# Kernel optimization log

Hardware: AMD Instinct MI355X
Metric: run time of the kernel (lower is better)

Reference implementation:

```python
import jax, jax.numpy as jnp
import numpy as np

ALPHA = 0.2  # LeakyReLU negative slope
NEG_BIG = -9e15

def setup_inputs() -> dict:
    key = jax.random.key(0)
    k1, k2, k3, k4, k5 = jax.random.split(key, 5)
    N, IN, OUT = 12288, 512, 256
    inp = jax.random.normal(k1, (N, IN), dtype=jnp.float32)
    adj = jax.random.randint(k2, (N, N), 0, 2, dtype=jnp.int32)
    # xavier_uniform with gain=1.414
    def xavier(k, shape, gain=1.414):
        fan_in, fan_out = shape[0], shape[1]
        bound = gain * np.sqrt(6.0 / (fan_in + fan_out))
        return jax.random.uniform(k, shape, dtype=jnp.float32, minval=-bound, maxval=bound)
    W = xavier(k3, (IN, OUT))
    a1 = xavier(k4, (OUT, 1))
    a2 = xavier(k5, (OUT, 1))
    return {"inp": inp, "adj": adj, "W": W, "a1": a1, "a2": a2}

def reference(inp, adj, W, a1, a2):
    h = inp @ W                      # [N, OUT]
    s1 = h @ a1                      # [N, 1]
    s2 = h @ a2                      # [N, 1]
    e = jax.nn.leaky_relu(s1 + s2.T, negative_slope=ALPHA)   # [N, N]
    scores = jnp.where(adj > 0, e, NEG_BIG)
    attention = jax.nn.softmax(scores, axis=1)               # row-wise softmax
    # dropout is identity in eval mode (training=False)
    h_prime = attention @ h          # [N, OUT]
    return jax.nn.elu(h_prime)       # concat=True -> elu
```

## Files before the change

kernel.cpp:

```cpp
#include <hip/hip_runtime.h>
#include <stdint.h>
#include <stddef.h>

#define NN    12288
#define INF   512
#define OUTF  256
#define ALPHA 0.2f
#define LOG2E 1.44269504088896340736f

typedef __attribute__((ext_vector_type(4))) float        f32x4;
typedef __attribute__((ext_vector_type(8))) short        bf16x8;
typedef __attribute__((ext_vector_type(4))) unsigned int u32x4;
typedef __attribute__((ext_vector_type(4))) int          i32x4;

static __device__ __forceinline__ unsigned short f2bf(float f) {
  union { float f; unsigned u; } v; v.f = f;
  unsigned r = v.u + 0x7fffu + ((v.u >> 16) & 1u);
  return (unsigned short)(r >> 16);
}
static __device__ __forceinline__ float bf2f(unsigned short s) {
  union { unsigned u; float f; } v; v.u = ((unsigned)s) << 16;
  return v.f;
}


__global__ __launch_bounds__(256) void k1_gemm_h(const float* __restrict__ inp,
                                                 const float* __restrict__ W,
                                                 unsigned short* __restrict__ hT) {
  __shared__ float inp_s[32][36];
  __shared__ float W_s[32][256];
  const int t = threadIdx.x;
  const int row0 = blockIdx.x * 32;
  const int tx = t & 63, ty = t >> 6;
  f32x4 acc[8];
#pragma unroll
  for (int r = 0; r < 8; ++r) acc[r] = f32x4{0.f, 0.f, 0.f, 0.f};
  for (int kc = 0; kc < 16; ++kc) {
    {
      const int r = t >> 3, ko = (t & 7) * 4;
      *(f32x4*)&inp_s[r][ko] = *(const f32x4*)(inp + (size_t)(row0 + r) * INF + kc * 32 + ko);
    }
#pragma unroll
    for (int j = 0; j < 8; ++j) {
      const int r = j * 4 + ty;
      *(f32x4*)&W_s[r][tx * 4] = *(const f32x4*)(W + (size_t)(kc * 32 + r) * OUTF + tx * 4);
    }
    __syncthreads();
#pragma unroll 4
    for (int k = 0; k < 32; ++k) {
      const f32x4 wv = *(const f32x4*)&W_s[k][tx * 4];
#pragma unroll
      for (int rr = 0; rr < 8; ++rr) acc[rr] += inp_s[ty * 8 + rr][k] * wv;
    }
    __syncthreads();
  }
#pragma unroll
  for (int rr = 0; rr < 8; ++rr) *(f32x4*)&W_s[ty * 8 + rr][tx * 4] = acc[rr];
  __syncthreads();
  {
    const int col = t;
    char* dst = (char*)hT + (size_t)col * (NN * 2) + (size_t)(row0 >> 6) * 128;
    const unsigned swz = (unsigned)((col & 7) << 4);
    const unsigned wbase = (unsigned)(row0 & 63) * 2;
#pragma unroll
    for (int s = 0; s < 4; ++s) {
      unsigned e0 = (unsigned)f2bf(W_s[s*8+0][col]) | ((unsigned)f2bf(W_s[s*8+1][col]) << 16);
      unsigned e1 = (unsigned)f2bf(W_s[s*8+2][col]) | ((unsigned)f2bf(W_s[s*8+3][col]) << 16);
      unsigned e2 = (unsigned)f2bf(W_s[s*8+4][col]) | ((unsigned)f2bf(W_s[s*8+5][col]) << 16);
      unsigned e3 = (unsigned)f2bf(W_s[s*8+6][col]) | ((unsigned)f2bf(W_s[s*8+7][col]) << 16);
      u32x4 p; p.x = e0; p.y = e1; p.z = e2; p.w = e3;
      *(u32x4*)(dst + ((wbase + (unsigned)s * 16) ^ swz)) = p;
    }
  }
}

__global__ __launch_bounds__(256) void k2_s12(const unsigned short* __restrict__ hT,
                                              const float* __restrict__ a1,
                                              const float* __restrict__ a2,
                                              float* __restrict__ s1,
                                              float* __restrict__ s2) {
  const int i = blockIdx.x * 256 + threadIdx.x;
  const size_t chunk = (size_t)(i >> 6) * 128;
  const unsigned within = (unsigned)(i & 63) * 2;
  float v1 = 0.f, v2 = 0.f;
  for (int d = 0; d < 256; ++d) {
    const unsigned off = within ^ ((unsigned)(d & 7) << 4);
    const unsigned short u =
        *(const unsigned short*)((const char*)hT + (size_t)d * (NN * 2) + chunk + off);
    const float f = bf2f(u);
    v1 += f * a1[d];
    v2 += f * a2[d];
  }
  s1[i] = v1; s2[i] = v2;
}

__global__ __launch_bounds__(256) void k3_s2max(const float* __restrict__ s2,
                                                float* __restrict__ s2max) {
  __shared__ float red[256];
  const int t = threadIdx.x;
  float m = -3.0e38f;
  for (int j = t; j < NN; j += 256) m = fmaxf(m, s2[j]);
  red[t] = m;
  __syncthreads();
  for (int s = 128; s > 0; s >>= 1) {
    if (t < s) red[t] = fmaxf(red[t], red[t + s]);
    __syncthreads();
  }
  if (t == 0) s2max[0] = red[0];
}

__global__ __launch_bounds__(256, 2) void k4_attn(const int* __restrict__ adj,
                                                  const unsigned short* __restrict__ hT,
                                                  const float* __restrict__ s1,
                                                  const float* __restrict__ s2,
                                                  const float* __restrict__ s2max,
                                                  float* __restrict__ accp,
                                                  float* __restrict__ denp) {
  __shared__ __align__(16) char B_lds[256 * 128];
  __shared__ __align__(16) char w_lds[64 * 128];
  const int t = threadIdx.x;
  const int w = t >> 6, l = t & 63;
  const int rb = blockIdx.x >> 1, half = blockIdx.x & 1;
  const int row0 = rb * 64;
  const int kstart = half * (NN / 2);

  const float S2MAX = s2max[0];
  const int wrow = w * 16 + (l >> 2);
  const int wrow_g = row0 + wrow;
  const int k0 = (l & 3) * 16;
  const float s1v = s1[wrow_g];
  const float tup = s1v + S2MAX;
  const float M = tup > 0.f ? tup : ALPHA * tup;
  float dsum = 0.f;

  f32x4 acc[4][4];
#pragma unroll
  for (int i = 0; i < 4; ++i)
#pragma unroll
    for (int j = 0; j < 4; ++j) acc[i][j] = f32x4{0.f, 0.f, 0.f, 0.f};

  const int* adjp = adj + (size_t)wrow_g * NN + kstart + k0;
  const float* s2p = s2 + kstart + k0;
  char* const wdst = w_lds + wrow * 128;
  const unsigned wswz = (unsigned)((wrow & 7) << 4);

  for (int it = 0; it < (NN / 2) / 64; ++it) {
    __syncthreads();
    {
      const size_t kb2 = (size_t)(kstart + it * 64) * 2;
#pragma unroll
      for (int s = 0; s < 8; ++s) {
        const int base = s * 256 + (w << 6);
        const int idx = base + l;
        const char* src = (const char*)hT + (size_t)(idx >> 3) * (NN * 2) + kb2 +
                          (size_t)(idx & 7) * 16;
        __builtin_amdgcn_global_load_lds(
            (const __attribute__((address_space(1))) unsigned int*)src,
            (__attribute__((address_space(3))) unsigned int*)(B_lds + (size_t)base * 16),
            16, 0, 0);
      }
    }
    {
      int aarr[16]; float sarr[16];
      *(i32x4*)(&aarr[0])  = *(const i32x4*)(adjp + 0);
      *(i32x4*)(&aarr[4])  = *(const i32x4*)(adjp + 4);
      *(i32x4*)(&aarr[8])  = *(const i32x4*)(adjp + 8);
      *(i32x4*)(&aarr[12]) = *(const i32x4*)(adjp + 12);
      *(f32x4*)(&sarr[0])  = *(const f32x4*)(s2p + 0);
      *(f32x4*)(&sarr[4])  = *(const f32x4*)(s2p + 4);
      *(f32x4*)(&sarr[8])  = *(const f32x4*)(s2p + 8);
      *(f32x4*)(&sarr[12]) = *(const f32x4*)(s2p + 12);
      unsigned pk[8];
#pragma unroll
      for (int q = 0; q < 8; ++q) {
        unsigned short us[2];
#pragma unroll
        for (int hh = 0; hh < 2; ++hh) {
          const int j = q * 2 + hh;
          const float tt = s1v + sarr[j];
          const float e = tt > 0.f ? tt : ALPHA * tt;
          float wv = 0.f;
          if (aarr[j] != 0) wv = exp2f((e - M) * LOG2E);
          us[hh] = f2bf(wv);
          dsum += bf2f(us[hh]);
        }
        pk[q] = (unsigned)us[0] | ((unsigned)us[1] << 16);
      }
      u32x4 p0; p0.x = pk[0]; p0.y = pk[1]; p0.z = pk[2]; p0.w = pk[3];
      u32x4 p1; p1.x = pk[4]; p1.y = pk[5]; p1.z = pk[6]; p1.w = pk[7];
      *(u32x4*)(wdst + (((unsigned)(k0 * 2)) ^ wswz)) = p0;
      *(u32x4*)(wdst + (((unsigned)(k0 * 2 + 16)) ^ wswz)) = p1;
      adjp += 64; s2p += 64;
    }
    __syncthreads();
#pragma unroll
    for (int kt = 0; kt < 2; ++kt) {
      const unsigned kbyte = (unsigned)((kt * 32 + (l >> 4) * 8) * 2);
      bf16x8 af[4], bfr[4];
#pragma unroll
      for (int rt = 0; rt < 4; ++rt) {
        const int row = rt * 16 + (l & 15);
        af[rt] = *(const bf16x8*)(w_lds + row * 128 + (kbyte ^ ((unsigned)((row & 7) << 4))));
      }
#pragma unroll
      for (int ct = 0; ct < 4; ++ct) {
        const int col = (w << 6) + ct * 16 + (l & 15);
        bfr[ct] = *(const bf16x8*)(B_lds + col * 128 + (kbyte ^ ((unsigned)((col & 7) << 4))));
      }
#pragma unroll
      for (int rt = 0; rt < 4; ++rt)
#pragma unroll
        for (int ct = 0; ct < 4; ++ct)
          acc[rt][ct] = __builtin_amdgcn_mfma_f32_16x16x32_bf16(af[rt], bfr[ct], acc[rt][ct],
                                                                0, 0, 0);
    }
  }
  dsum += __shfl_xor(dsum, 1);
  dsum += __shfl_xor(dsum, 2);
  if ((l & 3) == 0) denp[(size_t)half * NN + wrow_g] = dsum;
  float* ap = accp + (size_t)half * NN * OUTF;
#pragma unroll
  for (int rt = 0; rt < 4; ++rt) {
    const int row = row0 + rt * 16 + ((l >> 4) << 2);
#pragma unroll
    for (int ct = 0; ct < 4; ++ct) {
      const int col = (w << 6) + ct * 16 + (l & 15);
#pragma unroll
      for (int j = 0; j < 4; ++j)
        ap[(size_t)(row + j) * OUTF + col] = acc[rt][ct][j];
    }
  }
}

__global__ __launch_bounds__(256) void k5_combine(const float* __restrict__ accp,
                                                  const float* __restrict__ denp,
                                                  float* __restrict__ out) {
  const int idx = blockIdx.x * 256 + threadIdx.x;
  const int row = idx >> 6;
  const f32x4 a = *(const f32x4*)(accp + (size_t)idx * 4);
  const f32x4 b = *(const f32x4*)(accp + (size_t)NN * OUTF + (size_t)idx * 4);
  const float d = denp[row] + denp[NN + row];
  const float inv = 1.f / d;
  f32x4 v = (a + b) * inv;
  f32x4 r;
#pragma unroll
  for (int j = 0; j < 4; ++j) {
    const float x = v[j];
    r[j] = x > 0.f ? x : (__expf(x) - 1.f);
  }
  *(f32x4*)(out + (size_t)idx * 4) = r;
}

extern "C" void kernel_launch(void* const* d_in, const int* in_sizes, int n_in,
                              void* d_out, int out_size, void* d_ws, size_t ws_size,
                              hipStream_t stream) {
  const float* inp = (const float*)d_in[0];
  const int*   adj = (const int*)d_in[1];
  const float* W   = (const float*)d_in[2];
  const float* a1  = (const float*)d_in[3];
  const float* a2  = (const float*)d_in[4];
  float* out = (float*)d_out;
  char* ws = (char*)d_ws;

  unsigned short* hT  = (unsigned short*)(ws + 0);
  float* s1   = (float*)(ws + 6291456);
  float* s2   = (float*)(ws + 6340608);
  float* s2m  = (float*)(ws + 6389760);
  float* accp = (float*)(ws + 6390016);
  float* denp = (float*)(ws + 31555840);

  k1_gemm_h<<<dim3(NN / 32), dim3(256), 0, stream>>>(inp, W, hT);
  k2_s12<<<dim3(NN / 256), dim3(256), 0, stream>>>(hT, a1, a2, s1, s2);
  k3_s2max<<<dim3(1), dim3(256), 0, stream>>>(s2, s2m);
  k4_attn<<<dim3((NN / 64) * 2), dim3(256), 0, stream>>>(adj, hT, s1, s2, s2m, accp, denp);
  k5_combine<<<dim3(NN * OUTF / 1024), dim3(256), 0, stream>>>(accp, denp, out);
}
```

Baseline: 374.9 us.

## Double-buffer attention kernel with register-resident weights and 4-way K split

Restructures the attention kernel so each wave owns 32 rows and all 256 output columns. The attention weights are built directly in registers as MFMA A-fragments, so the LDS round trip for them disappears. hT tiles are double-buffered in LDS via global_load_lds, adjacency is prefetched one iteration ahead, s2 is cached in LDS, and there is a single barrier per step. The K dimension is split four ways when the workspace allows, to raise block count, at the cost of more partial-sum traffic in the combine kernel. The weights are now summed in fp32 before bf16 rounding.

```diff
diff --git a/kernel.cpp b/kernel.cpp
--- a/kernel.cpp
+++ b/kernel.cpp
@@ -109,6 +109,103 @@
   if (t == 0) s2max[0] = red[0];
 }
 
+
+#define GLDS16(SRC, DST)                                                        \
+  __builtin_amdgcn_global_load_lds(                                             \
+      (const __attribute__((address_space(1))) unsigned int*)(SRC),             \
+      (__attribute__((address_space(3))) unsigned int*)(DST), 16, 0, 0)
+
+#define K4_STAGE(BUF, IT)                                                       \
+  do {                                                                          \
+    const size_t _coff = (size_t)((kbase >> 6) + (IT)) * 128;                   \
+    _Pragma("unroll") for (int _p = 0; _p < 8; ++_p) {                          \
+      const int _idx = _p * 256 + t;                                            \
+      const char* _src = (const char*)hT + (size_t)(_idx >> 3) * (NN * 2) +     \
+                         _coff + (size_t)(_idx & 7) * 16;                       \
+      GLDS16(_src, (char*)B_lds + (size_t)(BUF) * 32768 +                       \
+                       (size_t)(_p * 256 + (wv << 6)) * 16);                    \
+    }                                                                           \
+  } while (0)
+
+#define K4_PREFETCH(DST, IT)                                                    \
+  do {                                                                          \
+    _Pragma("unroll") for (int _rt = 0; _rt < 2; ++_rt)                         \
+    _Pragma("unroll") for (int _kt = 0; _kt < 2; ++_kt) {                       \
+      const int* _p = adj + (size_t)(row0 + _rt * 16 + m) * NN +                \
+                      (kbase + (IT) * 64 + _kt * 32 + ko * 8);                  \
+      DST[_rt * 4 + _kt * 2 + 0] = *(const i32x4*)_p;                           \
+      DST[_rt * 4 + _kt * 2 + 1] = *(const i32x4*)(_p + 4);                     \
+    }                                                                           \
+  } while (0)
+
+#define K4_COMPUTE(AD, IT)                                                      \
+  do {                                                                          \
+    _Pragma("unroll") for (int _kt = 0; _kt < 2; ++_kt) {                       \
+      const f32x4 _sa = *(const f32x4*)(s2_lds + (IT) * 64 + _kt * 32 + ko * 8);\
+      const f32x4 _sb = *(const f32x4*)(s2_lds + (IT) * 64 + _kt * 32 + ko * 8 + 4);\
+      _Pragma("unroll") for (int _rt = 0; _rt < 2; ++_rt) {                     \
+        bf16x8 _f;                                                              \
+        _Pragma("unroll") for (int _j = 0; _j < 4; ++_j) {                      \
+          const float _tt = s1v[_rt] + _sa[_j];                                 \
+          const float _e = fmaxf(_tt, ALPHA * _tt);                             \
+          float _w = 0.f;                                                       \
+          if (AD[_rt * 4 + _kt * 2 + 0][_j] != 0)                               \
+            _w = exp2f(__builtin_fmaf(_e, LOG2E, -ML2[_rt]));                   \
+          dsum[_rt] += _w;                                                      \
+          _f[_j] = (short)f2bf(_w);                                             \
+        }                                                                       \
+        _Pragma("unroll") for (int _j = 0; _j < 4; ++_j) {                      \
+          const float _tt = s1v[_rt] + _sb[_j];                                 \
+          const float _e = fmaxf(_tt, ALPHA * _tt);                             \
+          float _w = 0.f;                                                       \
+          if (AD[_rt * 4 + _kt * 2 + 1][_j] != 0)                               \
+            _w = exp2f(__builtin_fmaf(_e, LOG2E, -ML2[_rt]));                   \
+          dsum[_rt] += _w;                                                      \
+          _f[4 + _j] = (short)f2bf(_w);                                         \
+        }                                                                       \
+        frag[_rt][_kt] = _f;                                                    \
+      }                                                                         \
+    }                                                                           \
+  } while (0)
+
+#define K4_MFMA(BUF)                                                            \
+  do {                                                                          \
+    const char* _Bb = (const char*)B_lds + (size_t)(BUF) * 32768;               \
+    _Pragma("unroll") for (int _kt = 0; _kt < 2; ++_kt) {                       \
+      const unsigned _kb = (unsigned)((_kt * 32 + ko * 8) * 2);                 \
+      _Pragma("unroll") for (int _ct = 0; _ct < 16; ++_ct) {                    \
+        const int _col = _ct * 16 + m;                                          \
+        const bf16x8 _b = *(const bf16x8*)(_Bb + _col * 128 +                   \
+                              (_kb ^ ((unsigned)((_col & 7) << 4))));           \
+        acc[0][_ct] = __builtin_amdgcn_mfma_f32_16x16x32_bf16(frag[0][_kt], _b, \
+                                                              acc[0][_ct], 0, 0, 0);\
+        acc[1][_ct] = __builtin_amdgcn_mfma_f32_16x16x32_bf16(frag[1][_kt], _b, \
+                                                              acc[1][_ct], 0, 0, 0);\
+      }                                                                         \
+    }                                                                           \
+  } while (0)
+
+#define K4_BARRIER()                                                            \
+  do {                                                                          \
+    asm volatile("s_waitcnt vmcnt(8)" ::: "memory");                            \
+    __builtin_amdgcn_sched_barrier(0);                                          \
+    __builtin_amdgcn_s_barrier();                                               \
+    __builtin_amdgcn_sched_barrier(0);                                          \
+  } while (0)
+
+#define K4_SUB(IT, BUF, ACUR, ANXT, ISLAST)                                     \
+  do {                                                                          \
+    if (!(ISLAST)) {                                                            \
+      K4_STAGE((BUF) ^ 1, (IT) + 1);                                            \
+      __builtin_amdgcn_sched_barrier(0);                                        \
+    }                                                                           \
+    K4_COMPUTE(ACUR, IT);                                                       \
+    if (!(ISLAST)) K4_PREFETCH(ANXT, (IT) + 1);                                 \
+    K4_MFMA(BUF);                                                               \
+    if (!(ISLAST)) K4_BARRIER();                                                \
+  } while (0)
+
+template <int KS>
 __global__ __launch_bounds__(256, 2) void k4_attn(const int* __restrict__ adj,
                                                   const unsigned short* __restrict__ hT,
                                                   const float* __restrict__ s1,
@@ -116,136 +213,96 @@
                                                   const float* __restrict__ s2max,
                                                   float* __restrict__ accp,
                                                   float* __restrict__ denp) {
-  __shared__ __align__(16) char B_lds[256 * 128];
-  __shared__ __align__(16) char w_lds[64 * 128];
+  constexpr int KRANGE = NN / KS;
+  constexpr int NIT = KRANGE / 64;
+  __shared__ __align__(16) char B_lds[2][256 * 128];
+  __shared__ __align__(16) float s2_lds[KRANGE];
   const int t = threadIdx.x;
-  const int w = t >> 6, l = t & 63;
-  const int rb = blockIdx.x >> 1, half = blockIdx.x & 1;
-  const int row0 = rb * 64;
-  const int kstart = half * (NN / 2);
+  const int wv = t >> 6, l = t & 63;
+  const int m = l & 15, ko = l >> 4;
+  const int rb = blockIdx.x / KS, part = blockIdx.x % KS;
+  const int row0 = rb * 128 + wv * 32;
+  const int kbase = part * KRANGE;
 
   const float S2MAX = s2max[0];
-  const int wrow = w * 16 + (l >> 2);
-  const int wrow_g = row0 + wrow;
-  const int k0 = (l & 3) * 16;
-  const float s1v = s1[wrow_g];
-  const float tup = s1v + S2MAX;
-  const float M = tup > 0.f ? tup : ALPHA * tup;
-  float dsum = 0.f;
-
-  f32x4 acc[4][4];
-#pragma unroll
-  for (int i = 0; i < 4; ++i)
-#pragma unroll
-    for (int j = 0; j < 4; ++j) acc[i][j] = f32x4{0.f, 0.f, 0.f, 0.f};
-
-  const int* adjp = adj + (size_t)wrow_g * NN + kstart + k0;
-  const float* s2p = s2 + kstart + k0;
-  char* const wdst = w_lds + wrow * 128;
-  const unsigned wswz = (unsigned)((wrow & 7) << 4);
-
-  for (int it = 0; it < (NN / 2) / 64; ++it) {
-    __syncthreads();
-    {
-      const size_t kb2 = (size_t)(kstart + it * 64) * 2;
-#pragma unroll
-      for (int s = 0; s < 8; ++s) {
-        const int base = s * 256 + (w << 6);
-        const int idx = base + l;
-        const char* src = (const char*)hT + (size_t)(idx >> 3) * (NN * 2) + kb2 +
-                          (size_t)(idx & 7) * 16;
-        __builtin_amdgcn_global_load_lds(
-            (const __attribute__((address_space(1))) unsigned int*)src,
-            (__attribute__((address_space(3))) unsigned int*)(B_lds + (size_t)base * 16),
-            16, 0, 0);
-      }
-    }
-    {
-      int aarr[16]; float sarr[16];
-      *(i32x4*)(&aarr[0])  = *(const i32x4*)(adjp + 0);
-      *(i32x4*)(&aarr[4])  = *(const i32x4*)(adjp + 4);
-      *(i32x4*)(&aarr[8])  = *(const i32x4*)(adjp + 8);
-      *(i32x4*)(&aarr[12]) = *(const i32x4*)(adjp + 12);
-      *(f32x4*)(&sarr[0])  = *(const f32x4*)(s2p + 0);
-      *(f32x4*)(&sarr[4])  = *(const f32x4*)(s2p + 4);
-      *(f32x4*)(&sarr[8])  = *(const f32x4*)(s2p + 8);
-      *(f32x4*)(&sarr[12]) = *(const f32x4*)(s2p + 12);
-      unsigned pk[8];
-#pragma unroll
-      for (int q = 0; q < 8; ++q) {
-        unsigned short us[2];
-#pragma unroll
-        for (int hh = 0; hh < 2; ++hh) {
-          const int j = q * 2 + hh;
-          const float tt = s1v + sarr[j];
-          const float e = tt > 0.f ? tt : ALPHA * tt;
-          float wv = 0.f;
-          if (aarr[j] != 0) wv = exp2f((e - M) * LOG2E);
-          us[hh] = f2bf(wv);
-          dsum += bf2f(us[hh]);
-        }
-        pk[q] = (unsigned)us[0] | ((unsigned)us[1] << 16);
-      }
-      u32x4 p0; p0.x = pk[0]; p0.y = pk[1]; p0.z = pk[2]; p0.w = pk[3];
-      u32x4 p1; p1.x = pk[4]; p1.y = pk[5]; p1.z = pk[6]; p1.w = pk[7];
-      *(u32x4*)(wdst + (((unsigned)(k0 * 2)) ^ wswz)) = p0;
-      *(u32x4*)(wdst + (((unsigned)(k0 * 2 + 16)) ^ wswz)) = p1;
-      adjp += 64; s2p += 64;
-    }
-    __syncthreads();
-#pragma unroll
-    for (int kt = 0; kt < 2; ++kt) {
-      const unsigned kbyte = (unsigned)((kt * 32 + (l >> 4) * 8) * 2);
-      bf16x8 af[4], bfr[4];
-#pragma unroll
-      for (int rt = 0; rt < 4; ++rt) {
-        const int row = rt * 16 + (l & 15);
-        af[rt] = *(const bf16x8*)(w_lds + row * 128 + (kbyte ^ ((unsigned)((row & 7) << 4))));
-      }
-#pragma unroll
-      for (int ct = 0; ct < 4; ++ct) {
-        const int col = (w << 6) + ct * 16 + (l & 15);
-        bfr[ct] = *(const bf16x8*)(B_lds + col * 128 + (kbyte ^ ((unsigned)((col & 7) << 4))));
-      }
-#pragma unroll
-      for (int rt = 0; rt < 4; ++rt)
-#pragma unroll
-        for (int ct = 0; ct < 4; ++ct)
-          acc[rt][ct] = __builtin_amdgcn_mfma_f32_16x16x32_bf16(af[rt], bfr[ct], acc[rt][ct],
-                                                                0, 0, 0);
-    }
-  }
-  dsum += __shfl_xor(dsum, 1);
-  dsum += __shfl_xor(dsum, 2);
-  if ((l & 3) == 0) denp[(size_t)half * NN + wrow_g] = dsum;
-  float* ap = accp + (size_t)half * NN * OUTF;
-#pragma unroll
-  for (int rt = 0; rt < 4; ++rt) {
-    const int row = row0 + rt * 16 + ((l >> 4) << 2);
-#pragma unroll
-    for (int ct = 0; ct < 4; ++ct) {
-      const int col = (w << 6) + ct * 16 + (l & 15);
+  float s1v[2], ML2[2], dsum[2];
+#pragma unroll
+  for (int rt = 0; rt < 2; ++rt) {
+    s1v[rt] = s1[row0 + rt * 16 + m];
+    const float tup = s1v[rt] + S2MAX;
+    const float M = fmaxf(tup, ALPHA * tup);
+    ML2[rt] = M * LOG2E;
+    dsum[rt] = 0.f;
+  }
+  f32x4 acc[2][16];
+#pragma unroll
+  for (int rt = 0; rt < 2; ++rt)
+#pragma unroll
+    for (int ct = 0; ct < 16; ++ct) acc[rt][ct] = f32x4{0.f, 0.f, 0.f, 0.f};
+
+  i32x4 adjE[8], adjO[8];
+  bf16x8 frag[2][2];
+
+  {
+    constexpr int S2CH = KRANGE / 1024;
+#pragma unroll
+    for (int p = 0; p < S2CH; ++p) {
+      const char* src = (const char*)(s2 + kbase) + (size_t)(p * 256 + t) * 16;
+      GLDS16(src, (char*)s2_lds + (size_t)(p * 256 + (wv << 6)) * 16);
+    }
+    K4_STAGE(0, 0);
+    __builtin_amdgcn_sched_barrier(0);
+    K4_PREFETCH(adjE, 0);
+    K4_BARRIER();
+  }
+
+  for (int it = 0; it < NIT - 2; it += 2) {
+    K4_SUB(it, 0, adjE, adjO, false);
+    K4_SUB(it + 1, 1, adjO, adjE, false);
+  }
+  K4_SUB(NIT - 2, 0, adjE, adjO, false);
+  K4_SUB(NIT - 1, 1, adjO, adjE, true);
+
+#pragma unroll
+  for (int rt = 0; rt < 2; ++rt) {
+    dsum[rt] += __shfl_xor(dsum[rt], 16);
+    dsum[rt] += __shfl_xor(dsum[rt], 32);
+  }
+  if (l < 16) {
+    denp[(size_t)part * NN + row0 + l] = dsum[0];
+    denp[(size_t)part * NN + row0 + 16 + l] = dsum[1];
+  }
+  float* ap = accp + (size_t)part * NN * OUTF;
+#pragma unroll
+  for (int rt = 0; rt < 2; ++rt)
+#pragma unroll
+    for (int ct = 0; ct < 16; ++ct) {
+      const int col = ct * 16 + m;
+      const int grow = row0 + rt * 16 + ko * 4;
 #pragma unroll
       for (int j = 0; j < 4; ++j)
-        ap[(size_t)(row + j) * OUTF + col] = acc[rt][ct][j];
-    }
-  }
-}
-
+        ap[(size_t)(grow + j) * OUTF + col] = acc[rt][ct][j];
+    }
+}
+
+template <int KS>
 __global__ __launch_bounds__(256) void k5_combine(const float* __restrict__ accp,
                                                   const float* __restrict__ denp,
                                                   float* __restrict__ out) {
   const int idx = blockIdx.x * 256 + threadIdx.x;
   const int row = idx >> 6;
-  const f32x4 a = *(const f32x4*)(accp + (size_t)idx * 4);
-  const f32x4 b = *(const f32x4*)(accp + (size_t)NN * OUTF + (size_t)idx * 4);
-  const float d = denp[row] + denp[NN + row];
-  const float inv = 1.f / d;
-  f32x4 v = (a + b) * inv;
+  f32x4 v = f32x4{0.f, 0.f, 0.f, 0.f};
+  float den = 0.f;
+#pragma unroll
+  for (int p = 0; p < KS; ++p) {
+    v += *(const f32x4*)(accp + (size_t)p * NN * OUTF + (size_t)idx * 4);
+    den += denp[(size_t)p * NN + row];
+  }
+  const float inv = 1.f / den;
   f32x4 r;
 #pragma unroll
   for (int j = 0; j < 4; ++j) {
-    const float x = v[j];
+    const float x = v[j] * inv;
     r[j] = x > 0.f ? x : (__expf(x) - 1.f);
   }
   *(f32x4*)(out + (size_t)idx * 4) = r;
@@ -262,16 +319,24 @@
   float* out = (float*)d_out;
   char* ws = (char*)d_ws;
 
-  unsigned short* hT  = (unsigned short*)(ws + 0);
-  float* s1   = (float*)(ws + 6291456);
-  float* s2   = (float*)(ws + 6340608);
-  float* s2m  = (float*)(ws + 6389760);
+  unsigned short* hT = (unsigned short*)(ws + 0);
+  float* s1  = (float*)(ws + 6291456);
+  float* s2  = (float*)(ws + 6340608);
+  float* s2m = (float*)(ws + 6389760);
   float* accp = (float*)(ws + 6390016);
-  float* denp = (float*)(ws + 31555840);
 
   k1_gemm_h<<<dim3(NN / 32), dim3(256), 0, stream>>>(inp, W, hT);
   k2_s12<<<dim3(NN / 256), dim3(256), 0, stream>>>(hT, a1, a2, s1, s2);
   k3_s2max<<<dim3(1), dim3(256), 0, stream>>>(s2, s2m);
-  k4_attn<<<dim3((NN / 64) * 2), dim3(256), 0, stream>>>(adj, hT, s1, s2, s2m, accp, denp);
-  k5_combine<<<dim3(NN * OUTF / 1024), dim3(256), 0, stream>>>(accp, denp, out);
-}
+
+  const size_t need4 = 6390016 + 4 * ((size_t)NN * OUTF * 4 + (size_t)NN * 4);
+  if (ws_size >= need4) {
+    float* denp = accp + 4 * (size_t)NN * OUTF;
+    k4_attn<4><<<dim3((NN / 128) * 4), dim3(256), 0, stream>>>(adj, hT, s1, s2, s2m, accp, denp);
+    k5_combine<4><<<dim3(NN * OUTF / 1024), dim3(256), 0, stream>>>(accp, denp, out);
+  } else {
+    float* denp = accp + 2 * (size_t)NN * OUTF;
+    k4_attn<2><<<dim3((NN / 128) * 2), dim3(256), 0, stream>>>(adj, hT, s1, s2, s2m, accp, denp);
+    k5_combine<2><<<dim3(NN * OUTF / 1024), dim3(256), 0, stream>>>(accp, denp, out);
+  }
+}
```

Result: slower. 484.3 us (+29.2%).
